# Performance work log

Measured on AMD Instinct MI355X. Metric: run time of the kernel, lower is better.

## Reference

```python
import jax, jax.numpy as jnp
import numpy as np
import math

B, T, D = 32, 336, 512
H = 8
HD = D // H
SEG_PER_DAY = 24
DAYS_PER_CYCLE = 7
NEG_INF = -1e30


def setup_inputs() -> dict:
    key = jax.random.key(0)
    ks = jax.random.split(key, 7)
    s = 1.0 / math.sqrt(D)
    x = jax.random.normal(ks[0], (B, T, D), dtype=jnp.float32)
    Wq = jax.random.uniform(ks[1], (D, D), minval=-s, maxval=s, dtype=jnp.float32)
    Wk = jax.random.uniform(ks[2], (D, D), minval=-s, maxval=s, dtype=jnp.float32)
    Wv = jax.random.uniform(ks[3], (D, D), minval=-s, maxval=s, dtype=jnp.float32)
    so = 1.0 / math.sqrt(2 * D)
    Wo = jax.random.uniform(ks[4], (2 * D, D), minval=-so, maxval=so, dtype=jnp.float32)
    bo = jax.random.uniform(ks[5], (D,), minval=-so, maxval=so, dtype=jnp.float32)
    random_bias = jax.random.normal(ks[6], (2, T, T), dtype=jnp.float32) * 0.01
    return {"x": x, "Wq": Wq, "Wk": Wk, "Wv": Wv, "Wo": Wo, "bo": bo,
            "random_bias": random_bias}


def reference(x, Wq, Wk, Wv, Wo, bo, random_bias):
    b, t, d = x.shape
    q = (x @ Wq).reshape(b, t, H, HD).transpose(0, 2, 1, 3)  # [b,h,t,hd]
    k = (x @ Wk).reshape(b, t, H, HD).transpose(0, 2, 1, 3)
    v = (x @ Wv).reshape(b, t, H, HD).transpose(0, 2, 1, 3)

    idx = jnp.arange(t)
    hour_ids = idx % SEG_PER_DAY
    day_ids = (idx // SEG_PER_DAY) % DAYS_PER_CYCLE
    hour_adj = hour_ids[:, None] == hour_ids[None, :]   # [t,t] bool
    day_adj = day_ids[:, None] == day_ids[None, :]

    # base QK^T scores computed once, reused for both granularities
    base = jnp.einsum('bhqd,bhkd->bhqk', q, k) / math.sqrt(HD)  # [b,h,t,t]

    def graph_attn(adj, bias):
        scores = base + bias[None, None]                      # additive bias
        scores = jnp.where(adj[None, None], scores, NEG_INF)  # periodic mask
        attn = jax.nn.softmax(scores, axis=-1)
        return jnp.einsum('bhqk,bhkd->bhqd', attn, v)

    hour_out = graph_attn(hour_adj, random_bias[0, :t, :t])
    day_out = graph_attn(day_adj, random_bias[1, :t, :t])

    hour_out = hour_out.transpose(0, 2, 1, 3).reshape(b, t, d)
    day_out = day_out.transpose(0, 2, 1, 3).reshape(b, t, d)
    combined = jnp.concatenate([hour_out, day_out], axis=-1)  # [b,t,2d]
    return combined @ Wo + bo
```

## Files before the change

### kernel.cpp

```cpp
#include <hip/hip_runtime.h>


typedef __attribute__((ext_vector_type(8))) __bf16 bf16x8;
typedef __attribute__((ext_vector_type(8))) unsigned short u16x8;
typedef __attribute__((ext_vector_type(4))) float f32x4;

__device__ __forceinline__ unsigned short f2bf(float f) {
  union { float f; unsigned u; } v; v.f = f;
  unsigned r = v.u + 0x7fffu + ((v.u >> 16) & 1u);
  return (unsigned short)(r >> 16);
}

__device__ __forceinline__ void load_lds16(const void* g, void* l) {
  __builtin_amdgcn_global_load_lds(
      (const __attribute__((address_space(1))) void*)g,
      (__attribute__((address_space(3))) void*)l, 16, 0, 0);
}

template <bool OUT_BF16>
__global__ __launch_bounds__(256) void gemm_bt(
    const unsigned short* __restrict__ A, const unsigned short* __restrict__ Bt,
    void* __restrict__ Cv, const float* __restrict__ bias, int M, int N, int K) {
  __shared__ __align__(16) unsigned short As[128 * 64];
  __shared__ __align__(16) unsigned short Bs[128 * 64];
  const int tid = threadIdx.x;
  const int lane = tid & 63;
  const int wid = tid >> 6;
  const int ntile = N >> 7;

  const int cpx = gridDim.x >> 3;
  const int bid = (blockIdx.x & 7) * cpx + (blockIdx.x >> 3);

  const int bx = bid % ntile;
  const int by = bid / ntile;
  const long row0 = (long)by << 7;
  const long col0 = (long)bx << 7;
  const int wr = (wid >> 1) << 6;
  const int wc = (wid & 1) << 6;

  const unsigned short* ag[4];
  const unsigned short* bg[4];
  int lofs[4];
#pragma unroll
  for (int it = 0; it < 4; ++it) {
    const int s = tid + (it << 8);
    const int r = s >> 3;
    const int ko = (s & 7) << 3;
    ag[it] = A + (row0 + r) * (long)K + ko;
    bg[it] = Bt + (col0 + r) * (long)K + ko;
    lofs[it] = s << 4;
  }

  f32x4 acc[4][4];
  const f32x4 zero = {0.f, 0.f, 0.f, 0.f};
#pragma unroll
  for (int m = 0; m < 4; ++m)
#pragma unroll
    for (int n = 0; n < 4; ++n) acc[m][n] = zero;

  const int fr = lane & 15;
  const int krow = (lane >> 4) << 3;

  for (int kk = 0; kk < K; kk += 64) {
#pragma unroll
    for (int it = 0; it < 4; ++it) {
      load_lds16(ag[it] + kk, (char*)As + lofs[it]);
      load_lds16(bg[it] + kk, (char*)Bs + lofs[it]);
    }
    __syncthreads();
#pragma unroll
    for (int ks = 0; ks < 2; ++ks) {
      bf16x8 a[4], b[4];
#pragma unroll
      for (int m = 0; m < 4; ++m)
        a[m] = *(const bf16x8*)(const void*)(As + (wr + m * 16 + fr) * 64 + ks * 32 + krow);
#pragma unroll
      for (int n = 0; n < 4; ++n)
        b[n] = *(const bf16x8*)(const void*)(Bs + (wc + n * 16 + fr) * 64 + ks * 32 + krow);
#pragma unroll
      for (int m = 0; m < 4; ++m)
#pragma unroll
        for (int n = 0; n < 4; ++n)
          acc[m][n] = __builtin_amdgcn_mfma_f32_16x16x32_bf16(a[m], b[n], acc[m][n], 0, 0, 0);
    }
    __syncthreads();
  }

  const int orow = (lane >> 4) << 2;
  const int ocol = lane & 15;
#pragma unroll
  for (int m = 0; m < 4; ++m) {
#pragma unroll
    for (int n = 0; n < 4; ++n) {
      const long gcol = col0 + wc + n * 16 + ocol;
      float bv = 0.f;
      if (!OUT_BF16 && bias) bv = bias[gcol];
#pragma unroll
      for (int r = 0; r < 4; ++r) {
        const long grow = row0 + wr + m * 16 + orow + r;
        const float val = acc[m][n][r] + bv;
        if (OUT_BF16)
          ((unsigned short*)Cv)[grow * N + gcol] = f2bf(val);
        else
          ((float*)Cv)[grow * N + gcol] = val;
      }
    }
  }
}

template <int MODE>
__device__ __forceinline__ void attn_body(
    const int cls, const int h, const int b, const int lane,
    const unsigned short* __restrict__ QKV, const float* __restrict__ bias,
    unsigned short* __restrict__ comb, unsigned short* smem) {
  constexpr int NQT = MODE ? 3 : 1;
  constexpr int NKT = MODE ? 3 : 1;
  constexpr int PVK = MODE ? 2 : 1;
  constexpr int MEM = MODE ? 48 : 14;
  constexpr int PLD = MODE ? 72 : 40;
  constexpr int VLD = MODE ? 72 : 40;
  constexpr int PE = 16 * NQT * PLD;
  constexpr int VE = 64 * VLD;

  unsigned short* P_lds = smem;
  unsigned short* Vt = smem + PE;
  const long rowBase = (long)b * 336;

  auto tmap = [&](int i) -> int {
    if (MODE) return 24 * cls + i + ((i < 24) ? 0 : 144);
    return cls + 24 * i;
  };

  {
    const uint4 z4 = {0u, 0u, 0u, 0u};
    uint4* p4 = (uint4*)P_lds;
#pragma unroll
    for (int i = 0; i < PE / 8 / 64 + 1; ++i) {
      const int idx = lane + i * 64;
      if (idx < PE / 8) p4[idx] = z4;
    }
    uint4* v4 = (uint4*)Vt;
#pragma unroll
    for (int i = 0; i < VE / 8 / 64 + 1; ++i) {
      const int idx = lane + i * 64;
      if (idx < VE / 8) v4[idx] = z4;
    }
  }
  __syncthreads();

  {
    const int kloc = lane >> 3;
    const int d0 = (lane & 7) * 8;
    constexpr int NPASS = (MEM + 7) / 8;
#pragma unroll
    for (int p = 0; p < NPASS; ++p) {
      const int k = p * 8 + kloc;
      if (k < MEM) {
        const long off = (rowBase + tmap(k)) * 1536 + 1024 + h * 64 + d0;
        const u16x8 vv = *(const u16x8*)(const void*)(QKV + off);
#pragma unroll
        for (int e = 0; e < 8; ++e) Vt[(d0 + e) * VLD + k] = vv[e];
      }
    }
  }

  const int fr = lane & 15;
  const int kgrp = (lane >> 4) << 3;
  bf16x8 aq[NQT][2], bk[NKT][2];
#pragma unroll
  for (int it = 0; it < NQT; ++it) {
    const int qi = 16 * it + fr;
    const long rq = (rowBase + tmap(qi < MEM ? qi : MEM - 1)) * 1536 + h * 64 + kgrp;
#pragma unroll
    for (int ks = 0; ks < 2; ++ks)
      aq[it][ks] = *(const bf16x8*)(const void*)(QKV + rq + ks * 32);
  }
#pragma unroll
  for (int jt = 0; jt < NKT; ++jt) {
    const int kj = 16 * jt + fr;
    const long rk = (rowBase + tmap(kj < MEM ? kj : MEM - 1)) * 1536 + 512 + h * 64 + kgrp;
#pragma unroll
    for (int ks = 0; ks < 2; ++ks)
      bk[jt][ks] = *(const bf16x8*)(const void*)(QKV + rk + ks * 32);
  }

  f32x4 sacc[NQT][NKT];
  const f32x4 zero = {0.f, 0.f, 0.f, 0.f};
#pragma unroll
  for (int it = 0; it < NQT; ++it)
#pragma unroll
    for (int jt = 0; jt < NKT; ++jt) sacc[it][jt] = zero;
#pragma unroll
  for (int ks = 0; ks < 2; ++ks)
#pragma unroll
    for (int it = 0; it < NQT; ++it)
#pragma unroll
      for (int jt = 0; jt < NKT; ++jt)
        sacc[it][jt] = __builtin_amdgcn_mfma_f32_16x16x32_bf16(aq[it][ks], bk[jt][ks], sacc[it][jt], 0, 0, 0);

  const int rgrp = (lane >> 4) << 2;
#pragma unroll
  for (int it = 0; it < NQT; ++it) {
#pragma unroll
    for (int r = 0; r < 4; ++r) {
      const int row = 16 * it + rgrp + r;
      const int tq = tmap(row < MEM ? row : MEM - 1);
      float sv[NKT];
#pragma unroll
      for (int jt = 0; jt < NKT; ++jt) {
        const int col = 16 * jt + fr;
        const int tk = tmap(col < MEM ? col : MEM - 1);
        sv[jt] = sacc[it][jt][r] * 0.125f + bias[(long)tq * 336 + tk];
        if (MODE == 0 && col >= MEM) sv[jt] = -1e30f;
      }
      float m = sv[0];
#pragma unroll
      for (int jt = 1; jt < NKT; ++jt) m = fmaxf(m, sv[jt]);
#pragma unroll
      for (int d = 1; d < 16; d <<= 1) m = fmaxf(m, __shfl_xor(m, d, 64));
      float e[NKT], sum = 0.f;
#pragma unroll
      for (int jt = 0; jt < NKT; ++jt) { e[jt] = __expf(sv[jt] - m); sum += e[jt]; }
#pragma unroll
      for (int d = 1; d < 16; d <<= 1) sum += __shfl_xor(sum, d, 64);
      const float inv = 1.f / sum;
#pragma unroll
      for (int jt = 0; jt < NKT; ++jt)
        P_lds[row * PLD + 16 * jt + fr] = f2bf(e[jt] * inv);
    }
  }
  __syncthreads();

  f32x4 oacc[NQT][4];
#pragma unroll
  for (int it = 0; it < NQT; ++it)
#pragma unroll
    for (int jt = 0; jt < 4; ++jt) oacc[it][jt] = zero;
#pragma unroll
  for (int ks = 0; ks < PVK; ++ks) {
    bf16x8 pa[NQT], vb[4];
#pragma unroll
    for (int it = 0; it < NQT; ++it)
      pa[it] = *(const bf16x8*)(const void*)(P_lds + (16 * it + fr) * PLD + ks * 32 + kgrp);
#pragma unroll
    for (int jt = 0; jt < 4; ++jt)
      vb[jt] = *(const bf16x8*)(const void*)(Vt + (16 * jt + fr) * VLD + ks * 32 + kgrp);
#pragma unroll
    for (int it = 0; it < NQT; ++it)
#pragma unroll
      for (int jt = 0; jt < 4; ++jt)
        oacc[it][jt] = __builtin_amdgcn_mfma_f32_16x16x32_bf16(pa[it], vb[jt], oacc[it][jt], 0, 0, 0);
  }

  const long colBase = (MODE ? 512 : 0) + h * 64;
#pragma unroll
  for (int it = 0; it < NQT; ++it) {
#pragma unroll
    for (int r = 0; r < 4; ++r) {
      const int row = 16 * it + rgrp + r;
      if (row < MEM) {
        const long base = (rowBase + tmap(row)) * 1024 + colBase;
#pragma unroll
        for (int jt = 0; jt < 4; ++jt)
          comb[base + 16 * jt + fr] = f2bf(oacc[it][jt][r]);
      }
    }
  }
}

__global__ __launch_bounds__(64) void attn_all(
    const unsigned short* __restrict__ QKV, const float* __restrict__ rb,
    unsigned short* __restrict__ comb) {
  __shared__ __align__(16) unsigned short smem[8064];
  const int lane = threadIdx.x & 63;
  const int bi = blockIdx.x;
  if (bi < 6144) {
    const int c = bi % 24;
    const int h = (bi / 24) & 7;
    const int b = bi / (24 * 8);
    attn_body<0>(c, h, b, lane, QKV, rb, comb, smem);
  } else {
    const int di = bi - 6144;
    const int dc = di % 7;
    const int h = (di / 7) & 7;
    const int b = di / 56;
    attn_body<1>(dc, h, b, lane, QKV, rb + 336 * 336, comb, smem);
  }
}

__global__ __launch_bounds__(256) void cast_all(
    const float* __restrict__ x, const float* __restrict__ Wq,
    const float* __restrict__ Wk, const float* __restrict__ Wv,
    const float* __restrict__ Wo, unsigned short* __restrict__ xb,
    unsigned short* __restrict__ WqkvT, unsigned short* __restrict__ WoT) {
  const int g0 = blockIdx.x * 256 + threadIdx.x;
  const int gsz = gridDim.x * 256;
  for (int i = g0; i < 1376256; i += gsz) {
    const float4 v = ((const float4*)x)[i];
    ushort4 o;
    o.x = f2bf(v.x); o.y = f2bf(v.y); o.z = f2bf(v.z); o.w = f2bf(v.w);
    ((ushort4*)xb)[i] = o;
  }
  for (int idx = g0; idx < 1536 * 512; idx += gsz) {
    const int n = idx >> 9, k = idx & 511;
    const float* W = (n < 512) ? Wq : ((n < 1024) ? Wk : Wv);
    WqkvT[idx] = f2bf(W[k * 512 + (n & 511)]);
  }
  for (int idx = g0; idx < 512 * 1024; idx += gsz) {
    const int n = idx >> 10, k = idx & 1023;
    WoT[idx] = f2bf(Wo[k * 512 + n]);
  }
}

extern "C" void kernel_launch(void* const* d_in, const int* in_sizes, int n_in,
                              void* d_out, int out_size, void* d_ws, size_t ws_size,
                              hipStream_t stream) {
  (void)in_sizes; (void)n_in; (void)out_size; (void)ws_size;
  const float* x  = (const float*)d_in[0];
  const float* Wq = (const float*)d_in[1];
  const float* Wk = (const float*)d_in[2];
  const float* Wv = (const float*)d_in[3];
  const float* Wo = (const float*)d_in[4];
  const float* bo = (const float*)d_in[5];
  const float* rb = (const float*)d_in[6];

  char* ws = (char*)d_ws;
  unsigned short* xbf   = (unsigned short*)(ws + 0);
  unsigned short* WqkvT = (unsigned short*)(ws + 11010048);
  unsigned short* WoT   = (unsigned short*)(ws + 12582912);
  unsigned short* QKVb  = (unsigned short*)(ws + 13631488);
  unsigned short* comb  = (unsigned short*)(ws + 46661632);

  cast_all<<<2048, 256, 0, stream>>>(x, Wq, Wk, Wv, Wo, xbf, WqkvT, WoT);

  gemm_bt<true><<<84 * 12, 256, 0, stream>>>(xbf, WqkvT, QKVb, nullptr, 10752, 1536, 512);

  attn_all<<<6144 + 1792, 64, 0, stream>>>(QKVb, rb, comb);

  gemm_bt<false><<<84 * 4, 256, 0, stream>>>(comb, WoT, d_out, bo, 10752, 512, 1024);
}
```

Measured before the change: 98.76 us.

## Swizzle GEMM LDS layout and use 64-row tiles for output projection

Applies an XOR swizzle to the 16-byte chunks written to LDS by global_load_lds, and to the matching fragment reads, so the MFMA operand loads avoid LDS bank conflicts. Also templates the GEMM on the row-tile size and launches the output projection with 64-row tiles, doubling its grid from 336 to 672 blocks to improve CU occupancy. The smaller tile lowers operand reuse per block in exchange for more parallelism.

```diff
diff --git a/kernel.cpp b/kernel.cpp
--- a/kernel.cpp
+++ b/kernel.cpp
@@ -17,11 +17,13 @@
       (__attribute__((address_space(3))) void*)l, 16, 0, 0);
 }
 
-template <bool OUT_BF16>
+template <bool OUT_BF16, int BM>
 __global__ __launch_bounds__(256) void gemm_bt(
     const unsigned short* __restrict__ A, const unsigned short* __restrict__ Bt,
     void* __restrict__ Cv, const float* __restrict__ bias, int M, int N, int K) {
-  __shared__ __align__(16) unsigned short As[128 * 64];
+  constexpr int MR = BM / 32;
+  constexpr int AIT = BM / 32;
+  __shared__ __align__(16) unsigned short As[BM * 64];
   __shared__ __align__(16) unsigned short Bs[128 * 64];
   const int tid = threadIdx.x;
   const int lane = tid & 63;
@@ -33,52 +35,66 @@
 
   const int bx = bid % ntile;
   const int by = bid / ntile;
-  const long row0 = (long)by << 7;
+  const long row0 = (long)by * BM;
   const long col0 = (long)bx << 7;
-  const int wr = (wid >> 1) << 6;
+  const int wr = (wid >> 1) * (BM >> 1);
   const int wc = (wid & 1) << 6;
 
-  const unsigned short* ag[4];
+  const unsigned short* ag[AIT];
   const unsigned short* bg[4];
-  int lofs[4];
+  int alofs[AIT], blofs[4];
+#pragma unroll
+  for (int it = 0; it < AIT; ++it) {
+    const int s = tid + (it << 8);
+    const int r = s >> 3;
+    const int c = s & 7;
+    ag[it] = A + (row0 + r) * (long)K + (((c ^ (r & 7)) << 3));
+    alofs[it] = s << 4;
+  }
 #pragma unroll
   for (int it = 0; it < 4; ++it) {
     const int s = tid + (it << 8);
     const int r = s >> 3;
-    const int ko = (s & 7) << 3;
-    ag[it] = A + (row0 + r) * (long)K + ko;
-    bg[it] = Bt + (col0 + r) * (long)K + ko;
-    lofs[it] = s << 4;
-  }
-
-  f32x4 acc[4][4];
+    const int c = s & 7;
+    bg[it] = Bt + (col0 + r) * (long)K + (((c ^ (r & 7)) << 3));
+    blofs[it] = s << 4;
+  }
+
+  f32x4 acc[MR][4];
   const f32x4 zero = {0.f, 0.f, 0.f, 0.f};
 #pragma unroll
-  for (int m = 0; m < 4; ++m)
+  for (int m = 0; m < MR; ++m)
 #pragma unroll
     for (int n = 0; n < 4; ++n) acc[m][n] = zero;
 
   const int fr = lane & 15;
-  const int krow = (lane >> 4) << 3;
+  const int grp = lane >> 4;
+  const int sw = fr & 7;
 
   for (int kk = 0; kk < K; kk += 64) {
 #pragma unroll
-    for (int it = 0; it < 4; ++it) {
-      load_lds16(ag[it] + kk, (char*)As + lofs[it]);
-      load_lds16(bg[it] + kk, (char*)Bs + lofs[it]);
-    }
+    for (int it = 0; it < AIT; ++it)
+      load_lds16(ag[it] + kk, (char*)As + alofs[it]);
+#pragma unroll
+    for (int it = 0; it < 4; ++it)
+      load_lds16(bg[it] + kk, (char*)Bs + blofs[it]);
     __syncthreads();
 #pragma unroll
     for (int ks = 0; ks < 2; ++ks) {
-      bf16x8 a[4], b[4];
-#pragma unroll
-      for (int m = 0; m < 4; ++m)
-        a[m] = *(const bf16x8*)(const void*)(As + (wr + m * 16 + fr) * 64 + ks * 32 + krow);
-#pragma unroll
-      for (int n = 0; n < 4; ++n)
-        b[n] = *(const bf16x8*)(const void*)(Bs + (wc + n * 16 + fr) * 64 + ks * 32 + krow);
-#pragma unroll
-      for (int m = 0; m < 4; ++m)
+      const int kc = ks * 4 + grp;
+      bf16x8 a[MR], b[4];
+#pragma unroll
+      for (int m = 0; m < MR; ++m) {
+        const int row = wr + m * 16 + fr;
+        a[m] = *(const bf16x8*)(const void*)(As + row * 64 + ((kc ^ sw) << 3));
+      }
+#pragma unroll
+      for (int n = 0; n < 4; ++n) {
+        const int row = wc + n * 16 + fr;
+        b[n] = *(const bf16x8*)(const void*)(Bs + row * 64 + ((kc ^ sw) << 3));
+      }
+#pragma unroll
+      for (int m = 0; m < MR; ++m)
 #pragma unroll
         for (int n = 0; n < 4; ++n)
           acc[m][n] = __builtin_amdgcn_mfma_f32_16x16x32_bf16(a[m], b[n], acc[m][n], 0, 0, 0);
@@ -89,7 +105,7 @@
   const int orow = (lane >> 4) << 2;
   const int ocol = lane & 15;
 #pragma unroll
-  for (int m = 0; m < 4; ++m) {
+  for (int m = 0; m < MR; ++m) {
 #pragma unroll
     for (int n = 0; n < 4; ++n) {
       const long gcol = col0 + wc + n * 16 + ocol;
@@ -333,9 +349,9 @@
 
   cast_all<<<2048, 256, 0, stream>>>(x, Wq, Wk, Wv, Wo, xbf, WqkvT, WoT);
 
-  gemm_bt<true><<<84 * 12, 256, 0, stream>>>(xbf, WqkvT, QKVb, nullptr, 10752, 1536, 512);
+  gemm_bt<true, 128><<<84 * 12, 256, 0, stream>>>(xbf, WqkvT, QKVb, nullptr, 10752, 1536, 512);
 
   attn_all<<<6144 + 1792, 64, 0, stream>>>(QKVb, rb, comb);
 
-  gemm_bt<false><<<84 * 4, 256, 0, stream>>>(comb, WoT, d_out, bo, 10752, 512, 1024);
-}
+  gemm_bt<false, 64><<<168 * 4, 256, 0, stream>>>(comb, WoT, d_out, bo, 10752, 512, 1024);
+}
```

Result: faster. 85.28 us (-13.7%).
